# Performance work log

Measured on AMD Instinct MI355X. Metric: run time of the kernel, lower is better.

Reference implementation:

```python
import jax, jax.numpy as jnp
import numpy as np

BS, NC, C, D = 8, 64, 256, 32
K, KB, ALPHA, B = 16, 8, 4, 16
HS, HM, HMOD = 64, 64, 32
N = NC * C
DLM = NC * D
MOD_IN = K + 3 * D + 1    # 113
MOD_OUT = K + KB + 1 + D  # 57


def setup_inputs() -> dict:
    key = jax.random.key(0)
    ks = jax.random.split(key, 12)
    rn = lambda k, s, sc=1.0: jax.random.normal(k, s, dtype=jnp.float32) * sc
    s_in, m_in = 3 * D + 1, 3 * D
    inp = {}
    inp['cc_signals_t'] = rn(ks[0], (BS, DLM))
    inp['h'] = rn(ks[1], (BS, NC, C, D), 0.1)
    inp['prev_messages'] = rn(ks[2], (BS, NC, C, D), 0.1)
    inp['decay_logit'] = jnp.zeros((BS, NC, C), jnp.float32)
    inp['primitives_state'] = jnp.zeros((BS, NC, C, D), jnp.float32)
    inp['hebbian_traces'] = jnp.zeros((BS, NC, C, K), jnp.float32)
    inp['state_w1'] = rn(ks[3], (HS, s_in), (2.0 / (s_in + HS)) ** 0.5)
    inp['state_b1'] = jnp.zeros((HS,), jnp.float32)
    inp['state_w2'] = rn(ks[4], (D, HS), (2.0 / (HS + D)) ** 0.5)
    inp['state_b2'] = jnp.zeros((D,), jnp.float32)
    inp['msg_w1'] = rn(ks[5], (HM, m_in), (2.0 / (m_in + HM)) ** 0.5)
    inp['msg_b1'] = jnp.zeros((HM,), jnp.float32)
    inp['msg_w2'] = rn(ks[6], (D, HM), (2.0 / (HM + D)) ** 0.5)
    inp['msg_b2'] = jnp.zeros((D,), jnp.float32)
    inp['mod_w1'] = rn(ks[7], (N, HMOD, MOD_IN), (2.0 / (MOD_IN + HMOD)) ** 0.5)
    inp['mod_b1'] = jnp.zeros((N, HMOD), jnp.float32)
    inp['mod_w2'] = rn(ks[8], (N, HMOD, MOD_OUT), (2.0 / (HMOD + MOD_OUT)) ** 0.5)
    inp['mod_b2'] = jnp.zeros((N, MOD_OUT), jnp.float32)
    inp['neuron_id'] = rn(ks[9], (NC, C, D), 1.0 / D ** 0.5)
    inp['conn_indices'] = jax.random.randint(ks[10], (NC, C, K), 0, C)
    inp['border_conn_indices'] = jax.random.randint(ks[11], (NC, B, KB), 0, NC * B)
    return inp


def reference(cc_signals_t, h, prev_messages, decay_logit, primitives_state,
              hebbian_traces, state_w1, state_b1, state_w2, state_b2,
              msg_w1, msg_b1, msg_w2, msg_b2,
              mod_w1, mod_b1, mod_w2, mod_b2, neuron_id,
              conn_indices, border_conn_indices):
    # ---- per-neuron modulator: each of N=NC*C neurons has unique MLP weights ----
    nid = jnp.broadcast_to(neuron_id[None], (BS, NC, C, D))
    mod_inp = jnp.concatenate(
        [hebbian_traces, h, decay_logit[..., None], primitives_state, nid], axis=-1)
    flat = mod_inp.reshape(BS, N, MOD_IN)
    hid = jnp.tanh(jnp.einsum('bni,nhi->bnh', flat, mod_w1) + mod_b1)
    out = (jnp.einsum('bnh,nho->bno', hid, mod_w2) + mod_b2).reshape(BS, NC, C, MOD_OUT)
    new_w_conn = out[..., :K]                          # [BS,NC,C,K]
    w_border = out[:, :, ALPHA:ALPHA + B, K:K + KB]    # border neurons only [BS,NC,B,KB]
    new_decay = out[..., K + KB]                       # [BS,NC,C]
    new_prim = out[..., K + KB + 1:]                   # [BS,NC,C,D]

    # ---- intra-cell weighted neighbor gather (irregular gather) ----
    cell = jnp.arange(NC)[:, None, None]
    neighbor = prev_messages[:, cell, conn_indices]    # [BS,NC,C,K,D]
    received = jnp.einsum('bnckd,bnck->bncd', neighbor, jax.nn.sigmoid(new_w_conn))

    # ---- inter-cell border gather over global border neuron pool ----
    border_msgs = prev_messages[:, :, ALPHA:ALPHA + B, :].reshape(BS, NC * B, D)
    nb = border_msgs[:, border_conn_indices]           # [BS,NC,B,KB,D]
    recv_border = jnp.einsum('bnjkd,bnjk->bnjd', nb, jax.nn.sigmoid(w_border))
    received = received.at[:, :, ALPHA:ALPHA + B, :].add(recv_border)

    # ---- inject external signal into the first ALPHA neurons of each cell ----
    inj = cc_signals_t.reshape(BS, NC, 1, D)
    received = received.at[:, :, :ALPHA, :].add(
        jnp.broadcast_to(inj, (BS, NC, ALPHA, D)))

    # ---- decay-gated state update through shared state MLP ----
    primitives_new = primitives_state + new_prim
    decay = jax.nn.sigmoid(new_decay)[..., None]       # [BS,NC,C,1]
    s_in = jnp.concatenate([h, received, primitives_new, decay], axis=-1)  # 3D+1
    sh = jnp.tanh(jnp.einsum('...i,hi->...h', s_in, state_w1) + state_b1)
    dh = jnp.einsum('...h,dh->...d', sh, state_w2) + state_b2
    h_new = decay * h + (1.0 - decay) * jnp.tanh(dh)

    # ---- shared message MLP ----
    m_in = jnp.concatenate([h_new, received, nid], axis=-1)  # 3D
    mh = jnp.tanh(jnp.einsum('...i,hi->...h', m_in, msg_w1) + msg_b1)
    msg = jnp.tanh(jnp.einsum('...h,dh->...d', mh, msg_w2) + msg_b2)

    # ---- hebbian trace EMA: pre/post message correlation per connection ----
    nb_new = msg[:, cell, conn_indices]                # [BS,NC,C,K,D]
    corr = jnp.einsum('bncd,bnckd->bnck', msg, nb_new) / D
    hebbian_new = 0.9 * hebbian_traces + 0.1 * corr

    # ---- readout: mean over last ALPHA (readout) neurons per cell ----
    readout = msg[:, :, C - ALPHA:, :].mean(axis=2).reshape(BS, DLM)
    return readout, h_new, msg, hebbian_new
```

## Files before the change

kernel.cpp:

```cpp
#include <hip/hip_runtime.h>
#include <cstdint>
#include <cstddef>

constexpr int kBS = 8;
constexpr int kNC = 64;
constexpr int kC = 256;
constexpr int kD = 32;
constexpr int kK = 16;
constexpr int kKB = 8;
constexpr int kALPHA = 4;
constexpr int kB = 16;
constexpr int kHS = 64;
constexpr int kHM = 64;
constexpr int kHMOD = 32;
constexpr int kN = kNC * kC;
constexpr int kMODIN = kK + 3 * kD + 1;
constexpr int kMODOUT = kK + kKB + 1 + kD;
constexpr int kXS = 116;
constexpr int kWS = 116;
constexpr int kSLAB = 36;
constexpr int kW2TS = 36;

constexpr size_t kO1 = (size_t)kBS * kNC * kD;
constexpr size_t kO2 = kO1 + (size_t)kBS * kN * kD;
constexpr size_t kO3 = kO2 + (size_t)kBS * kN * kD;

__device__ __forceinline__ float sigmoidf_(float x) {
    return 1.0f / (1.0f + __expf(-x));
}

__global__ __launch_bounds__(256) void mod_mlp_kernel(
    const float* __restrict__ heb, const float* __restrict__ h,
    const float* __restrict__ dlog, const float* __restrict__ prim,
    const float* __restrict__ nid,
    const float* __restrict__ mw1, const float* __restrict__ mb1,
    const float* __restrict__ mw2, const float* __restrict__ mb2,
    float* __restrict__ modout, int mos, int poff)
{
    const int n = blockIdx.x;
    const int tid = threadIdx.x;

    __shared__ __align__(16) float xw[kBS * kXS];
    __shared__ __align__(16) float w1s[kHMOD * kWS];
    __shared__ __align__(16) float w2s[kHMOD * kMODOUT];
    __shared__ float hids[kBS * kHMOD];

    {
        const float4* w1g4 = (const float4*)(mw1 + (size_t)n * (kHMOD * kMODIN));
        #pragma unroll
        for (int r = 0; r < 4; ++r) {
            int t = tid + 256 * r;
            if (t < (kHMOD * kMODIN) / 4) {
                float4 v = w1g4[t];
                int f = t << 2;
                #pragma unroll
                for (int e = 0; e < 4; ++e) {
                    int fe = f + e;
                    int row = fe / kMODIN;
                    int col = fe - row * kMODIN;
                    float val = (e == 0) ? v.x : (e == 1) ? v.y : (e == 2) ? v.z : v.w;
                    w1s[row * kWS + col] = val;
                }
            }
        }
    }
    {
        const float4* w2g4 = (const float4*)(mw2 + (size_t)n * (kHMOD * kMODOUT));
        #pragma unroll
        for (int r = 0; r < 2; ++r) {
            int t = tid + 256 * r;
            if (t < (kHMOD * kMODOUT) / 4)
                *(float4*)&w2s[t << 2] = w2g4[t];
        }
    }
    {
        if (tid < kBS * kK) {
            int b = tid >> 4, i = tid & 15;
            xw[b * kXS + i] = heb[((size_t)b * kN + n) * kK + i];
        }
        {
            int b = tid >> 5, d = tid & 31;
            xw[b * kXS + 16 + d] = h[((size_t)b * kN + n) * kD + d];
            xw[b * kXS + 49 + d] = prim[((size_t)b * kN + n) * kD + d];
            xw[b * kXS + 81 + d] = nid[(size_t)n * kD + d];
        }
        if (tid < kBS)
            xw[tid * kXS + 48] = dlog[(size_t)tid * kN + n];
    }
    __syncthreads();

    {
        const int hh = tid & 31;
        const int b  = tid >> 5;
        const float* wr = w1s + hh * kWS;
        const float* xr = xw + b * kXS;
        float acc = mb1[(size_t)n * kHMOD + hh];
        #pragma unroll 4
        for (int q = 0; q < 28; ++q) {
            float4 wv = *(const float4*)(wr + 4*q);
            float4 xv = *(const float4*)(xr + 4*q);
            acc += wv.x*xv.x + wv.y*xv.y + wv.z*xv.z + wv.w*xv.w;
        }
        acc += wr[112] * xr[112];
        hids[b * kHMOD + hh] = tanhf(acc);
    }
    __syncthreads();

    for (int t = tid; t < kBS * kMODOUT; t += 256) {
        int b2 = t / kMODOUT;
        int o  = t - b2 * kMODOUT;
        const float* hr = hids + b2 * kHMOD;
        float acc = mb2[(size_t)n * kMODOUT + o];
        #pragma unroll
        for (int hx = 0; hx < kHMOD; ++hx)
            acc += hr[hx] * w2s[hx * kMODOUT + o];
        int oo = (o < 25) ? o : (o + (poff - 25));
        modout[((size_t)b2 * kN + n) * mos + oo] = acc;
    }
}

__global__ __launch_bounds__(256) void cell_kernel(
    const float* __restrict__ cc, const float* __restrict__ hin,
    const float* __restrict__ pmsg, const float* __restrict__ prim,
    const float* __restrict__ hebin, const float* __restrict__ nid,
    const float* __restrict__ sw1, const float* __restrict__ sb1,
    const float* __restrict__ sw2, const float* __restrict__ sb2,
    const float* __restrict__ mw1g, const float* __restrict__ mb1g,
    const float* __restrict__ mw2g, const float* __restrict__ mb2g,
    const int* __restrict__ conn, const int* __restrict__ bconn,
    const float* __restrict__ modout, float* __restrict__ out,
    int mos, int poff)
{
    const int nc = blockIdx.x;
    const int b  = blockIdx.y;
    const int c  = threadIdx.x;

    __shared__ __align__(16) float slab[kC * kSLAB];
    __shared__ __align__(16) float w2ts[kHS * kW2TS];
    __shared__ __align__(16) float mw2ts[kHM * kW2TS];

    const size_t cellrow = ((size_t)b * kNC + nc) * kC;
    const size_t nbase   = cellrow + c;

    for (int idx = c; idx < kHS * kD; idx += kC) {
        int o2 = idx >> 6, h2 = idx & 63;
        w2ts[h2 * kW2TS + o2] = sw2[idx];
    }
    for (int idx = c; idx < kHM * kD; idx += kC) {
        int o2 = idx >> 6, h2 = idx & 63;
        mw2ts[h2 * kW2TS + o2] = mw2g[idx];
    }

    {
        const float4* s4 = (const float4*)(pmsg + cellrow * kD);
        for (int i = c; i < (kC * kD) / 4; i += kC) {
            float4 v = s4[i];
            *(float4*)&slab[(i >> 3) * kSLAB + ((i & 7) << 2)] = v;
        }
    }

    float hreg[32];
    {
        const float4* src = (const float4*)(hin + nbase * kD);
        #pragma unroll
        for (int q = 0; q < 8; ++q) {
            float4 v = src[q];
            hreg[4*q] = v.x; hreg[4*q+1] = v.y; hreg[4*q+2] = v.z; hreg[4*q+3] = v.w;
        }
    }
    const float* mo = modout + nbase * mos;
    float wcon[16];
    #pragma unroll
    for (int k = 0; k < 16; ++k) wcon[k] = sigmoidf_(mo[k]);
    int jreg[16];
    {
        const int4* cr = (const int4*)(conn + ((size_t)nc * kC + c) * kK);
        #pragma unroll
        for (int q = 0; q < 4; ++q) {
            int4 v = cr[q];
            jreg[4*q] = v.x; jreg[4*q+1] = v.y; jreg[4*q+2] = v.z; jreg[4*q+3] = v.w;
        }
    }
    const float decay = sigmoidf_(mo[kK + kKB]);
    float pnew[32];
    {
        const float4* p4 = (const float4*)(prim + nbase * kD);
        const int pbase = poff;
        #pragma unroll
        for (int q = 0; q < 8; ++q) {
            float4 v = p4[q];
            pnew[4*q]   = v.x + mo[pbase + 4*q];
            pnew[4*q+1] = v.y + mo[pbase + 4*q + 1];
            pnew[4*q+2] = v.z + mo[pbase + 4*q + 2];
            pnew[4*q+3] = v.w + mo[pbase + 4*q + 3];
        }
    }
    __syncthreads();

    float recv[32];
    #pragma unroll
    for (int d = 0; d < 32; ++d) recv[d] = 0.f;
    #pragma unroll 1
    for (int k = 0; k < 16; ++k) {
        const float4* row = (const float4*)(slab + jreg[k] * kSLAB);
        const float w = wcon[k];
        #pragma unroll
        for (int q = 0; q < 8; ++q) {
            float4 v = row[q];
            recv[4*q]   += v.x * w;
            recv[4*q+1] += v.y * w;
            recv[4*q+2] += v.z * w;
            recv[4*q+3] += v.w * w;
        }
    }
    if (c >= kALPHA && c < kALPHA + kB) {
        const int j = c - kALPHA;
        const int* br = bconn + ((size_t)nc * kB + j) * kKB;
        #pragma unroll 1
        for (int kb = 0; kb < kKB; ++kb) {
            int g = br[kb];
            int nc2 = g >> 4;
            int c2 = kALPHA + (g & 15);
            const float4* src = (const float4*)(pmsg + (((size_t)b * kNC + nc2) * kC + c2) * kD);
            float w = sigmoidf_(mo[kK + kb]);
            #pragma unroll
            for (int q = 0; q < 8; ++q) {
                float4 v = src[q];
                recv[4*q]   += v.x * w;
                recv[4*q+1] += v.y * w;
                recv[4*q+2] += v.z * w;
                recv[4*q+3] += v.w * w;
            }
        }
    }
    if (c < kALPHA) {
        const float* src = cc + (size_t)b * (kNC * kD) + nc * kD;
        #pragma unroll
        for (int d = 0; d < 32; ++d) recv[d] += src[d];
    }

    float dh[32];
    #pragma unroll
    for (int o = 0; o < 32; ++o) dh[o] = sb2[o];
    #pragma unroll 2
    for (int hh = 0; hh < kHS; ++hh) {
        const float* w = sw1 + hh * (3 * kD + 1);
        float acc = sb1[hh] + decay * w[96];
        #pragma unroll
        for (int i = 0; i < 32; ++i) acc += hreg[i] * w[i];
        #pragma unroll
        for (int i = 0; i < 32; ++i) acc += recv[i] * w[32 + i];
        #pragma unroll
        for (int i = 0; i < 32; ++i) acc += pnew[i] * w[64 + i];
        const float s = tanhf(acc);
        const float4* w2r = (const float4*)(w2ts + hh * kW2TS);
        #pragma unroll
        for (int q = 0; q < 8; ++q) {
            float4 wv = w2r[q];
            dh[4*q]   += s * wv.x;
            dh[4*q+1] += s * wv.y;
            dh[4*q+2] += s * wv.z;
            dh[4*q+3] += s * wv.w;
        }
    }
    float hnew[32];
    #pragma unroll
    for (int d = 0; d < 32; ++d) hnew[d] = decay * hreg[d] + (1.f - decay) * tanhf(dh[d]);

    {
        float4* dst = (float4*)(out + kO1 + nbase * kD);
        #pragma unroll
        for (int q = 0; q < 8; ++q)
            dst[q] = make_float4(hnew[4*q], hnew[4*q+1], hnew[4*q+2], hnew[4*q+3]);
    }

    float nidr[32];
    {
        const float4* src = (const float4*)(nid + ((size_t)nc * kC + c) * kD);
        #pragma unroll
        for (int q = 0; q < 8; ++q) {
            float4 v = src[q];
            nidr[4*q] = v.x; nidr[4*q+1] = v.y; nidr[4*q+2] = v.z; nidr[4*q+3] = v.w;
        }
    }
    float mm[32];
    #pragma unroll
    for (int o = 0; o < 32; ++o) mm[o] = mb2g[o];
    #pragma unroll 2
    for (int hh = 0; hh < kHM; ++hh) {
        const float* w = mw1g + hh * (3 * kD);
        float acc = mb1g[hh];
        #pragma unroll
        for (int i = 0; i < 32; ++i) acc += hnew[i] * w[i];
        #pragma unroll
        for (int i = 0; i < 32; ++i) acc += recv[i] * w[32 + i];
        #pragma unroll
        for (int i = 0; i < 32; ++i) acc += nidr[i] * w[64 + i];
        const float s = tanhf(acc);
        const float4* w2r = (const float4*)(mw2ts + hh * kW2TS);
        #pragma unroll
        for (int q = 0; q < 8; ++q) {
            float4 wv = w2r[q];
            mm[4*q]   += s * wv.x;
            mm[4*q+1] += s * wv.y;
            mm[4*q+2] += s * wv.z;
            mm[4*q+3] += s * wv.w;
        }
    }
    float msgr[32];
    #pragma unroll
    for (int d = 0; d < 32; ++d) msgr[d] = tanhf(mm[d]);

    __syncthreads();
    {
        float4* row = (float4*)(slab + c * kSLAB);
        #pragma unroll
        for (int q = 0; q < 8; ++q)
            row[q] = make_float4(msgr[4*q], msgr[4*q+1], msgr[4*q+2], msgr[4*q+3]);
    }
    __syncthreads();

    {
        const float* hb = hebin + nbase * kK;
        float* dst = out + kO3 + nbase * kK;
        #pragma unroll 1
        for (int k = 0; k < 16; ++k) {
            const float4* row = (const float4*)(slab + jreg[k] * kSLAB);
            float dot = 0.f;
            #pragma unroll
            for (int q = 0; q < 8; ++q) {
                float4 v = row[q];
                dot += msgr[4*q] * v.x + msgr[4*q+1] * v.y
                     + msgr[4*q+2] * v.z + msgr[4*q+3] * v.w;
            }
            dst[k] = 0.9f * hb[k] + 0.1f * (dot * (1.0f / 32.0f));
        }
    }
    {
        float4* dst = (float4*)(out + kO2 + cellrow * kD);
        for (int i = c; i < (kC * kD) / 4; i += kC)
            dst[i] = *(const float4*)&slab[(i >> 3) * kSLAB + ((i & 7) << 2)];
    }
    if (c < kD) {
        float s = 0.25f * (slab[(kC-4)*kSLAB + c] + slab[(kC-3)*kSLAB + c] +
                           slab[(kC-2)*kSLAB + c] + slab[(kC-1)*kSLAB + c]);
        out[(size_t)b * (kNC * kD) + nc * kD + c] = s;
    }
}

extern "C" void kernel_launch(void* const* d_in, const int* in_sizes, int n_in,
                              void* d_out, int out_size, void* d_ws, size_t ws_size,
                              hipStream_t stream)
{
    const float* cc    = (const float*)d_in[0];
    const float* h     = (const float*)d_in[1];
    const float* pmsg  = (const float*)d_in[2];
    const float* dlog  = (const float*)d_in[3];
    const float* prim  = (const float*)d_in[4];
    const float* heb   = (const float*)d_in[5];
    const float* sw1   = (const float*)d_in[6];
    const float* sb1   = (const float*)d_in[7];
    const float* sw2   = (const float*)d_in[8];
    const float* sb2   = (const float*)d_in[9];
    const float* mw1   = (const float*)d_in[10];
    const float* mb1   = (const float*)d_in[11];
    const float* mw2   = (const float*)d_in[12];
    const float* mb2   = (const float*)d_in[13];
    const float* modw1 = (const float*)d_in[14];
    const float* modb1 = (const float*)d_in[15];
    const float* modw2 = (const float*)d_in[16];
    const float* modb2 = (const float*)d_in[17];
    const float* nid   = (const float*)d_in[18];
    const int*   conn  = (const int*)d_in[19];
    const int*   bconn = (const int*)d_in[20];
    float* out = (float*)d_out;
    float* modout = (float*)d_ws;

    int mos = 57, poff = 25;
    if (ws_size >= (size_t)kBS * kN * 60 * sizeof(float)) { mos = 60; poff = 28; }

    mod_mlp_kernel<<<kN, 256, 0, stream>>>(heb, h, dlog, prim, nid,
                                           modw1, modb1, modw2, modb2,
                                           modout, mos, poff);
    cell_kernel<<<dim3(kNC, kBS), kC, 0, stream>>>(cc, h, pmsg, prim, heb, nid,
                                                   sw1, sb1, sw2, sb2,
                                                   mw1, mb1, mw2, mb2,
                                                   conn, bconn, modout, out,
                                                   mos, poff);
}
```

Measured before the change: 729.1 us.

## Map one wavefront per neuron in modulator MLP, split dot-product accumulators

The per-neuron modulator kernel now assigns one 64-lane wavefront to each neuron, four neurons per block, so it needs no block-wide __syncthreads. Inputs are held in registers and each layer-1 dot product is split across two lane halves that are combined with a shuffle. Layer-2 weights are read straight from global memory into per-lane registers rather than staged through shared memory. The cell kernel's MLP dot products use four independent partial sums to shorten the dependent FMA chains, which changes floating-point summation order and adds register pressure.

Measured after the change: 712.9 us. 2.2% less time.

```diff
diff --git a/kernel.cpp b/kernel.cpp
--- a/kernel.cpp
+++ b/kernel.cpp
@@ -17,7 +17,6 @@
 constexpr int kMODIN = kK + 3 * kD + 1;
 constexpr int kMODOUT = kK + kKB + 1 + kD;
 constexpr int kXS = 116;
-constexpr int kWS = 116;
 constexpr int kSLAB = 36;
 constexpr int kW2TS = 36;
 
@@ -37,85 +36,103 @@
     const float* __restrict__ mw2, const float* __restrict__ mb2,
     float* __restrict__ modout, int mos, int poff)
 {
-    const int n = blockIdx.x;
-    const int tid = threadIdx.x;
-
-    __shared__ __align__(16) float xw[kBS * kXS];
-    __shared__ __align__(16) float w1s[kHMOD * kWS];
-    __shared__ __align__(16) float w2s[kHMOD * kMODOUT];
-    __shared__ float hids[kBS * kHMOD];
+    const int wv = threadIdx.x >> 6;
+    const int lane = threadIdx.x & 63;
+    const int n = (blockIdx.x << 2) | wv;
+
+    __shared__ __align__(16) float xs[4][kBS * kXS];
+    __shared__ __align__(16) float w1sh[4][kHMOD * kXS];
+    __shared__ __align__(16) float hs[4][kBS * kHMOD];
+    float* xw  = xs[wv];
+    float* w1s = w1sh[wv];
+    float* hid = hs[wv];
 
     {
         const float4* w1g4 = (const float4*)(mw1 + (size_t)n * (kHMOD * kMODIN));
+        for (int t = lane; t < (kHMOD * kMODIN) / 4; t += 64) {
+            float4 v = w1g4[t];
+            int f = t << 2;
+            #pragma unroll
+            for (int e = 0; e < 4; ++e) {
+                int fe = f + e;
+                int r = fe / kMODIN;
+                int c = fe - r * kMODIN;
+                float val = (e == 0) ? v.x : (e == 1) ? v.y : (e == 2) ? v.z : v.w;
+                w1s[r * kXS + c] = val;
+            }
+        }
+    }
+    {
+        {
+            int t = lane;          int b0 = t >> 4,  i0 = t & 15;
+            xw[b0 * kXS + i0] = heb[((size_t)b0 * kN + n) * kK + i0];
+            t += 64;               int b1 = t >> 4,  i1 = t & 15;
+            xw[b1 * kXS + i1] = heb[((size_t)b1 * kN + n) * kK + i1];
+        }
         #pragma unroll
         for (int r = 0; r < 4; ++r) {
-            int t = tid + 256 * r;
-            if (t < (kHMOD * kMODIN) / 4) {
-                float4 v = w1g4[t];
-                int f = t << 2;
-                #pragma unroll
-                for (int e = 0; e < 4; ++e) {
-                    int fe = f + e;
-                    int row = fe / kMODIN;
-                    int col = fe - row * kMODIN;
-                    float val = (e == 0) ? v.x : (e == 1) ? v.y : (e == 2) ? v.z : v.w;
-                    w1s[row * kWS + col] = val;
-                }
-            }
-        }
-    }
-    {
-        const float4* w2g4 = (const float4*)(mw2 + (size_t)n * (kHMOD * kMODOUT));
-        #pragma unroll
-        for (int r = 0; r < 2; ++r) {
-            int t = tid + 256 * r;
-            if (t < (kHMOD * kMODOUT) / 4)
-                *(float4*)&w2s[t << 2] = w2g4[t];
-        }
-    }
-    {
-        if (tid < kBS * kK) {
-            int b = tid >> 4, i = tid & 15;
-            xw[b * kXS + i] = heb[((size_t)b * kN + n) * kK + i];
-        }
-        {
-            int b = tid >> 5, d = tid & 31;
+            int t = lane + 64 * r;
+            int b = t >> 5, d = t & 31;
             xw[b * kXS + 16 + d] = h[((size_t)b * kN + n) * kD + d];
             xw[b * kXS + 49 + d] = prim[((size_t)b * kN + n) * kD + d];
             xw[b * kXS + 81 + d] = nid[(size_t)n * kD + d];
         }
-        if (tid < kBS)
-            xw[tid * kXS + 48] = dlog[(size_t)tid * kN + n];
-    }
-    __syncthreads();
-
-    {
-        const int hh = tid & 31;
-        const int b  = tid >> 5;
-        const float* wr = w1s + hh * kWS;
-        const float* xr = xw + b * kXS;
-        float acc = mb1[(size_t)n * kHMOD + hh];
-        #pragma unroll 4
-        for (int q = 0; q < 28; ++q) {
-            float4 wv = *(const float4*)(wr + 4*q);
-            float4 xv = *(const float4*)(xr + 4*q);
-            acc += wv.x*xv.x + wv.y*xv.y + wv.z*xv.z + wv.w*xv.w;
-        }
-        acc += wr[112] * xr[112];
-        hids[b * kHMOD + hh] = tanhf(acc);
-    }
-    __syncthreads();
-
-    for (int t = tid; t < kBS * kMODOUT; t += 256) {
-        int b2 = t / kMODOUT;
-        int o  = t - b2 * kMODOUT;
-        const float* hr = hids + b2 * kHMOD;
-        float acc = mb2[(size_t)n * kMODOUT + o];
+        if (lane < kBS)
+            xw[lane * kXS + 48] = dlog[(size_t)lane * kN + n];
+    }
+
+    const int b    = lane >> 3;
+    const int half = (lane >> 2) & 1;
+    const int hq   = lane & 3;
+
+    float4 xr[14];
+    {
+        const float* xbase = xw + b * kXS + half * 56;
+        #pragma unroll
+        for (int q = 0; q < 14; ++q)
+            xr[q] = *(const float4*)(xbase + 4 * q);
+    }
+    const float x112 = (half == 1) ? xw[b * kXS + 112] : 0.0f;
+
+    #pragma unroll
+    for (int s = 0; s < 8; ++s) {
+        const int hh = (s << 2) + hq;
+        const float* wrow = w1s + hh * kXS + half * 56;
+        float p0 = 0.f, p1 = 0.f, p2 = 0.f, p3 = 0.f;
+        #pragma unroll
+        for (int q = 0; q < 14; ++q) {
+            float4 wv4 = *(const float4*)(wrow + 4 * q);
+            p0 += wv4.x * xr[q].x; p1 += wv4.y * xr[q].y;
+            p2 += wv4.z * xr[q].z; p3 += wv4.w * xr[q].w;
+        }
+        float acc = ((p0 + p1) + (p2 + p3)) + w1s[hh * kXS + 112] * x112;
+        acc += __shfl_xor(acc, 4, 64);
+        const float hv = tanhf(acc + mb1[(size_t)n * kHMOD + hh]);
+        if (half == 0) hid[b * kHMOD + hh] = hv;
+    }
+
+    const int o = (lane < kMODOUT) ? lane : (kMODOUT - 1);
+    float w2c[kHMOD];
+    {
+        const float* w2g = mw2 + (size_t)n * (kHMOD * kMODOUT) + o;
         #pragma unroll
         for (int hx = 0; hx < kHMOD; ++hx)
-            acc += hr[hx] * w2s[hx * kMODOUT + o];
-        int oo = (o < 25) ? o : (o + (poff - 25));
-        modout[((size_t)b2 * kN + n) * mos + oo] = acc;
+            w2c[hx] = w2g[hx * kMODOUT];
+    }
+    const float bo = mb2[(size_t)n * kMODOUT + o];
+    const int oo = (o < 25) ? o : (o + (poff - 25));
+    #pragma unroll
+    for (int b2 = 0; b2 < kBS; ++b2) {
+        const float4* h4 = (const float4*)(hid + b2 * kHMOD);
+        float acc = bo;
+        #pragma unroll
+        for (int j = 0; j < 8; ++j) {
+            float4 hv = h4[j];
+            acc += hv.x * w2c[4*j] + hv.y * w2c[4*j+1]
+                 + hv.z * w2c[4*j+2] + hv.w * w2c[4*j+3];
+        }
+        if (lane < kMODOUT)
+            modout[((size_t)b2 * kN + n) * mos + oo] = acc;
     }
 }
 
@@ -245,13 +262,29 @@
     #pragma unroll 2
     for (int hh = 0; hh < kHS; ++hh) {
         const float* w = sw1 + hh * (3 * kD + 1);
-        float acc = sb1[hh] + decay * w[96];
-        #pragma unroll
-        for (int i = 0; i < 32; ++i) acc += hreg[i] * w[i];
-        #pragma unroll
-        for (int i = 0; i < 32; ++i) acc += recv[i] * w[32 + i];
-        #pragma unroll
-        for (int i = 0; i < 32; ++i) acc += pnew[i] * w[64 + i];
+        float p0 = 0.f, p1 = 0.f, p2 = 0.f, p3 = 0.f;
+        #pragma unroll
+        for (int q = 0; q < 8; ++q) {
+            p0 += hreg[4*q+0] * w[4*q+0];
+            p1 += hreg[4*q+1] * w[4*q+1];
+            p2 += hreg[4*q+2] * w[4*q+2];
+            p3 += hreg[4*q+3] * w[4*q+3];
+        }
+        #pragma unroll
+        for (int q = 0; q < 8; ++q) {
+            p0 += recv[4*q+0] * w[32 + 4*q+0];
+            p1 += recv[4*q+1] * w[32 + 4*q+1];
+            p2 += recv[4*q+2] * w[32 + 4*q+2];
+            p3 += recv[4*q+3] * w[32 + 4*q+3];
+        }
+        #pragma unroll
+        for (int q = 0; q < 8; ++q) {
+            p0 += pnew[4*q+0] * w[64 + 4*q+0];
+            p1 += pnew[4*q+1] * w[64 + 4*q+1];
+            p2 += pnew[4*q+2] * w[64 + 4*q+2];
+            p3 += pnew[4*q+3] * w[64 + 4*q+3];
+        }
+        float acc = sb1[hh] + decay * w[96] + ((p0 + p1) + (p2 + p3));
         const float s = tanhf(acc);
         const float4* w2r = (const float4*)(w2ts + hh * kW2TS);
         #pragma unroll
@@ -289,14 +322,29 @@
     #pragma unroll 2
     for (int hh = 0; hh < kHM; ++hh) {
         const float* w = mw1g + hh * (3 * kD);
-        float acc = mb1g[hh];
-        #pragma unroll
-        for (int i = 0; i < 32; ++i) acc += hnew[i] * w[i];
-        #pragma unroll
-        for (int i = 0; i < 32; ++i) acc += recv[i] * w[32 + i];
-        #pragma unroll
-        for (int i = 0; i < 32; ++i) acc += nidr[i] * w[64 + i];
-        const float s = tanhf(acc);
+        float p0 = 0.f, p1 = 0.f, p2 = 0.f, p3 = 0.f;
+        #pragma unroll
+        for (int q = 0; q < 8; ++q) {
+            p0 += hnew[4*q+0] * w[4*q+0];
+            p1 += hnew[4*q+1] * w[4*q+1];
+            p2 += hnew[4*q+2] * w[4*q+2];
+            p3 += hnew[4*q+3] * w[4*q+3];
+        }
+        #pragma unroll
+        for (int q = 0; q < 8; ++q) {
+            p0 += recv[4*q+0] * w[32 + 4*q+0];
+            p1 += recv[4*q+1] * w[32 + 4*q+1];
+            p2 += recv[4*q+2] * w[32 + 4*q+2];
+            p3 += recv[4*q+3] * w[32 + 4*q+3];
+        }
+        #pragma unroll
+        for (int q = 0; q < 8; ++q) {
+            p0 += nidr[4*q+0] * w[64 + 4*q+0];
+            p1 += nidr[4*q+1] * w[64 + 4*q+1];
+            p2 += nidr[4*q+2] * w[64 + 4*q+2];
+            p3 += nidr[4*q+3] * w[64 + 4*q+3];
+        }
+        const float s = tanhf(mb1g[hh] + ((p0 + p1) + (p2 + p3)));
         const float4* w2r = (const float4*)(mw2ts + hh * kW2TS);
         #pragma unroll
         for (int q = 0; q < 8; ++q) {
@@ -379,9 +427,9 @@
     int mos = 57, poff = 25;
     if (ws_size >= (size_t)kBS * kN * 60 * sizeof(float)) { mos = 60; poff = 28; }
 
-    mod_mlp_kernel<<<kN, 256, 0, stream>>>(heb, h, dlog, prim, nid,
-                                           modw1, modb1, modw2, modb2,
-                                           modout, mos, poff);
+    mod_mlp_kernel<<<kN / 4, 256, 0, stream>>>(heb, h, dlog, prim, nid,
+                                               modw1, modb1, modw2, modb2,
+                                               modout, mos, poff);
     cell_kernel<<<dim3(kNC, kBS), kC, 0, stream>>>(cc, h, pmsg, prim, heb, nid,
                                                    sw1, sb1, sw2, sb2,
                                                    mw1, mb1, mw2, mb2,
```
